# Kernel optimization log

Measured on AMD Instinct MI355X. Metric: run time of the kernel, lower is better.

The kernel has to match this reference:

```python
import jax, jax.numpy as jnp
import numpy as np

BATCH, IN, HID, OMID, OUT = 8192, 64, 1024, 128, 1
MAX_ITER = 8
EPS = 1e-3


def setup_inputs() -> dict:
    key = jax.random.key(0)
    ks = jax.random.split(key, 32)
    s_in, s_h = 1.0 / np.sqrt(IN), 1.0 / np.sqrt(HID)
    d = {"x": jax.random.normal(ks[0], (BATCH, IN), jnp.float32)}
    names = ["i", "f", "c", "o"]
    for j, n in enumerate(names):
        d[f"Wx{n}"] = jax.random.uniform(ks[1 + 4 * j], (HID, IN), jnp.float32, -s_in, s_in)
        d[f"bx{n}"] = jax.random.uniform(ks[2 + 4 * j], (HID,), jnp.float32, -s_in, s_in)
        d[f"Wh{n}"] = jax.random.uniform(ks[3 + 4 * j], (HID, HID), jnp.float32, -s_h, s_h)
        d[f"bh{n}"] = jax.random.uniform(ks[4 + 4 * j], (HID,), jnp.float32, -s_h, s_h)
    d["W_halt"] = jax.random.uniform(ks[20], (1, HID), jnp.float32, -s_h, s_h)
    d["b_halt"] = jax.random.uniform(ks[21], (1,), jnp.float32, -s_h, s_h)
    d["W1"] = jax.random.uniform(ks[22], (OMID, HID), jnp.float32, -s_h, s_h)
    d["b1"] = jax.random.uniform(ks[23], (OMID,), jnp.float32, -s_h, s_h)
    s_m = 1.0 / np.sqrt(OMID)
    d["W2"] = jax.random.uniform(ks[24], (OUT, OMID), jnp.float32, -s_m, s_m)
    d["b2"] = jax.random.uniform(ks[25], (OUT,), jnp.float32, -s_m, s_m)
    return d


def _act_forward(x, Wxi, bxi, Whi, bhi, Wxf, bxf, Whf, bhf, Wxc, bxc, Whc, bhc,
                 Wxo, bxo, Who, bho, W_halt, b_halt, W1, b1, W2, b2):
    B = x.shape[0]
    state0 = jnp.zeros((B, HID), x.dtype)
    cell0 = jnp.zeros((B, HID), x.dtype)
    p0 = jnp.zeros((B,), x.dtype)
    active0 = jnp.ones((B,), bool)

    def step(carry, t):
        state, cell, p_sum, active = carry
        # four LSTM-style gates (computed dense; masked update == torch's gather/scatter)
        i_g = jax.nn.sigmoid(x @ Wxi.T + bxi + state @ Whi.T + bhi)
        f_g = jax.nn.sigmoid(x @ Wxf.T + bxf + state @ Whf.T + bhf)
        c_g = jnp.tanh(x @ Wxc.T + bxc + state @ Whc.T + bhc)
        o_g = jax.nn.sigmoid(x @ Wxo.T + bxo + state @ Who.T + bho)
        am = active[:, None]
        cell = jnp.where(am, f_g * cell + i_g * c_g, cell)
        state = jnp.where(am, o_g * jnp.tanh(cell), state)
        out = jax.nn.sigmoid(jax.nn.relu(state @ W1.T + b1) @ W2.T + b2)  # (B, OUT)
        h = jax.nn.sigmoid(state @ W_halt.T + b_halt)[:, 0]               # (B,)
        p_new = p_sum + h
        last = t == MAX_ITER - 1
        finished = active & ((p_new >= 1.0 - EPS) | last)
        halt_rec = jnp.where(finished, 1.0 - p_sum, jnp.where(active, h, 0.0))
        p_sum = jnp.where(finished, 1.0, jnp.where(active, p_new, p_sum))
        out_rec = jnp.where(am, out, 0.0)
        active = active & ~finished
        return (state, cell, p_sum, active), (out_rec, halt_rec)

    _, (outs, halts) = jax.lax.scan(step, (state0, cell0, p0, active0), jnp.arange(MAX_ITER))
    # outs: (T, B, OUT), halts: (T, B); final = sum_t out_t * p_halt_t
    return jnp.einsum("tbo,tb->bo", outs, halts)


def reference(x, Wxi, bxi, Whi, bhi, Wxf, bxf, Whf, bhf, Wxc, bxc, Whc, bhc,
              Wxo, bxo, Who, bho, W_halt, b_halt, W1, b1, W2, b2):
    return _act_forward(x, Wxi, bxi, Whi, bhi, Wxf, bxf, Whf, bhf, Wxc, bxc, Whc, bhc,
                        Wxo, bxo, Who, bho, W_halt, b_halt, W1, b1, W2, b2)
```

## Files before the change

### kernel.cpp

```cpp
#include <hip/hip_runtime.h>
#include <hip/hip_bf16.h>

#define BATCH 8192
#define IN_DIM 64
#define HID 1024
#define KTOT 1088
#define NGATES 4096
#define OMID 128
#define NP 256
#define MAX_ITER 8

#define TM 128
#define TN 128
#define TK 64
#define GTM 256
#define GTN 256
#define TAILB 64

typedef __attribute__((ext_vector_type(8))) short short8;
typedef __attribute__((ext_vector_type(4))) float float4v;

__device__ __forceinline__ float bf2f(short s) {
    union { float f; unsigned u; } v; v.u = ((unsigned)(unsigned short)s) << 16; return v.f;
}
__device__ __forceinline__ short f2bf(float f) {
    union { float f; unsigned u; } v; v.f = f;
    unsigned r = v.u + 0x7fff + ((v.u >> 16) & 1);
    return (short)(r >> 16);
}
__device__ __forceinline__ float sigmoidf_(float x) {
    float xc = fminf(fmaxf(x, -30.f), 30.f);
    return 1.f / (1.f + __expf(-xc));
}
__device__ __forceinline__ float tanhf_(float x) {
    float xc = fminf(fmaxf(x, -15.f), 15.f);
    float e = __expf(2.f * xc);
    return (e - 1.f) / (e + 1.f);
}
__device__ __forceinline__ int aload(const int* p) {
    return __hip_atomic_load((int*)p, __ATOMIC_RELAXED, __HIP_MEMORY_SCOPE_AGENT);
}
__device__ __forceinline__ void astore(int* p, int v) {
    __hip_atomic_store(p, v, __ATOMIC_RELAXED, __HIP_MEMORY_SCOPE_AGENT);
}

__device__ __forceinline__ void gbar(int* bar, int phase, int tid) {
    __syncthreads();
    if (tid == 0) {
        __threadfence();
        __hip_atomic_fetch_add(bar, 1, __ATOMIC_ACQ_REL, __HIP_MEMORY_SCOPE_AGENT);
        while (aload(bar) < TAILB * phase)
            __builtin_amdgcn_s_sleep(8);
        __threadfence();
    }
    __syncthreads();
}

__device__ __forceinline__ void gates_epilogue(
    const float4v (&acc)[4][4], int m0, int bx, int wave, int lane, int first,
    const float* __restrict__ bias_g, float* __restrict__ cell,
    short* __restrict__ Sout, const int* __restrict__ ridx, int n_act)
{
    const int wm = wave & 1, wn = wave >> 1;
    const int colq = lane & 15, q = lane >> 4;
    const int G = bx * 2 + wn;
    const int h = G * 16 + colq;
    const float bi  = bias_g[G * 64 +  0 + colq];
    const float bff = bias_g[G * 64 + 16 + colq];
    const float bc  = bias_g[G * 64 + 32 + colq];
    const float bo  = bias_g[G * 64 + 48 + colq];
#pragma unroll
    for (int i = 0; i < 4; ++i) {
        const int pbase = m0 + wm * 64 + i * 16 + q * 4;
#pragma unroll
        for (int r = 0; r < 4; ++r) {
            const int pos = pbase + r;
            if (pos < n_act) {
                const int row = ridx[pos];
                const float ig = sigmoidf_(acc[i][0][r] + bi);
                const float fg = sigmoidf_(acc[i][1][r] + bff);
                const float cg = tanhf_(acc[i][2][r] + bc);
                const float og = sigmoidf_(acc[i][3][r] + bo);
                const size_t ci = (size_t)row * HID + h;
                const float c = first ? (ig * cg) : (fg * cell[ci] + ig * cg);
                cell[ci] = c;
                Sout[(size_t)row * HID + h] = f2bf(og * tanhf_(c));
            }
        }
    }
}

__global__ __launch_bounds__(512, 1) void gates_k(
    const short* __restrict__ S, const short* __restrict__ XB,
    const short* __restrict__ B,
    const float* __restrict__ bias_g, int nK, int hidK, int first,
    float* __restrict__ cell, short* __restrict__ Sout,
    const int* __restrict__ ridx, const int* __restrict__ cnt, int t)
{
    __shared__ short As[2][GTM * TK];
    __shared__ short Bs[2][GTN * TK];
    const int n_act = cnt[t];
    const int tid  = threadIdx.x;
    const int wave = tid >> 6, lane = tid & 63;
    const int wm2 = wave >> 2, wn4 = wave & 3;
    const int colq = lane & 15, q = lane >> 4;
    const int lrow8 = lane >> 3;
    const int lk    = (((lane & 7) ^ lrow8) * 8);
    const int xq = colq & 7;
    const int abase = (wm2 * 128 + colq) * TK;
    const int bbase = (wn4 * 64  + colq) * TK;

    int bx, byS;
    {
        const int lin  = (int)blockIdx.x + 16 * (int)blockIdx.y;
        const int xcd  = lin & 7;
        const int slot = lin >> 3;
        bx  = (xcd & 1) * 8 + (slot & 7);
        byS = (xcd >> 1) * 4 + (slot >> 3);
    }
    const int n0 = bx * GTN;

    for (int by = byS; by * GTM < n_act; by += 16) {
        const int m0 = by * GTM;

        int rows_[4];
        const short* gb[4];
#pragma unroll
        for (int it = 0; it < 4; ++it) {
            const int rr = wave * 32 + it * 8 + lrow8;
            rows_[it] = ridx[m0 + rr];
            gb[it] = B + (size_t)(n0 + rr) * KTOT + lk;
        }

        float4v acc[8][4];
#pragma unroll
        for (int i = 0; i < 8; ++i)
#pragma unroll
            for (int j = 0; j < 4; ++j) acc[i][j] = (float4v)0.f;

        auto stage = [&](int ki, int buf) {
            const int kk = ki * TK;
            const bool fromS = (kk < hidK);
#pragma unroll
            for (int it = 0; it < 4; ++it) {
                const int dst = (wave * 32 + it * 8) * TK;
                const short* sa = fromS
                    ? (S  + (size_t)rows_[it] * HID    + kk + lk)
                    : (XB + (size_t)rows_[it] * IN_DIM + lk);
                __builtin_amdgcn_global_load_lds(
                    (const __attribute__((address_space(1))) void*)sa,
                    (__attribute__((address_space(3))) void*)(As[buf] + dst), 16, 0, 0);
                __builtin_amdgcn_global_load_lds(
                    (const __attribute__((address_space(1))) void*)(gb[it] + kk),
                    (__attribute__((address_space(3))) void*)(Bs[buf] + dst), 16, 0, 0);
            }
        };

        stage(0, 0);
        if (nK > 1) {
            stage(1, 1);
            asm volatile("s_waitcnt vmcnt(16)" ::: "memory");
        } else {
            asm volatile("s_waitcnt vmcnt(0)" ::: "memory");
        }
        asm volatile("s_barrier" ::: "memory");

        for (int ki = 0; ki < nK; ++ki) {
            const int cur = ki & 1;
            const short* Ac = As[cur];
            const short* Bc = Bs[cur];
#pragma unroll
            for (int c2 = 0; c2 < 2; ++c2) {
                const int xt = ((q + 4 * c2) ^ xq) << 3;
                short8 af[8], bf[4];
#pragma unroll
                for (int i = 0; i < 8; ++i)
                    af[i] = *(const short8*)(Ac + abase + i * (16 * TK) + xt);
#pragma unroll
                for (int j = 0; j < 4; ++j)
                    bf[j] = *(const short8*)(Bc + bbase + j * (16 * TK) + xt);
#pragma unroll
                for (int i = 0; i < 8; ++i)
#pragma unroll
                    for (int j = 0; j < 4; ++j)
                        acc[i][j] = __builtin_amdgcn_mfma_f32_16x16x32_bf16(af[i], bf[j], acc[i][j], 0, 0, 0);
            }
            asm volatile("s_waitcnt lgkmcnt(0)" ::: "memory");
            asm volatile("s_barrier" ::: "memory");
            if (ki + 2 < nK) {
                stage(ki + 2, cur);
                asm volatile("s_waitcnt vmcnt(16)" ::: "memory");
                asm volatile("s_barrier" ::: "memory");
            } else if (ki + 1 < nK) {
                asm volatile("s_waitcnt vmcnt(0)" ::: "memory");
                asm volatile("s_barrier" ::: "memory");
            }
        }

        const int G = bx * 4 + wn4;
        const int h = G * 16 + colq;
        const float bi  = bias_g[G * 64 +  0 + colq];
        const float bff = bias_g[G * 64 + 16 + colq];
        const float bc  = bias_g[G * 64 + 32 + colq];
        const float bo  = bias_g[G * 64 + 48 + colq];
#pragma unroll
        for (int i = 0; i < 8; ++i) {
            const int pbase = m0 + wm2 * 128 + i * 16 + q * 4;
#pragma unroll
            for (int r = 0; r < 4; ++r) {
                const int pos = pbase + r;
                if (pos < n_act) {
                    const int row = ridx[pos];
                    const float ig = sigmoidf_(acc[i][0][r] + bi);
                    const float fg = sigmoidf_(acc[i][1][r] + bff);
                    const float cg = tanhf_(acc[i][2][r] + bc);
                    const float og = sigmoidf_(acc[i][3][r] + bo);
                    const size_t ci = (size_t)row * HID + h;
                    const float c = first ? (ig * cg) : (fg * cell[ci] + ig * cg);
                    cell[ci] = c;
                    Sout[(size_t)row * HID + h] = f2bf(og * tanhf_(c));
                }
            }
        }
    }
}

__device__ __forceinline__ void gates_tile(
    short* As, short* Bs, int tid,
    const short* __restrict__ S, const short* __restrict__ XB,
    const short* __restrict__ B,
    const float* __restrict__ bias_g,
    float* __restrict__ cell, short* __restrict__ Sout,
    const int* __restrict__ ridx, int n_act, int m0, int bx)
{
    const int wave = tid >> 6, lane = tid & 63;
    const int wm = wave & 1, wn = wave >> 1;
    const int colq = lane & 15, q = lane >> 4;
    const int lrow8 = lane >> 3;
    const int lk    = (((lane & 7) ^ lrow8) * 8);
    const int n0 = bx * TN;

    int aoff[4][2], boff[4][2];
#pragma unroll
    for (int i = 0; i < 4; ++i) {
        const int Ra = wm * 64 + i * 16 + colq;
        const int Rb = wn * 64 + i * 16 + colq;
#pragma unroll
        for (int c2 = 0; c2 < 2; ++c2) {
            const int C = q + 4 * c2;
            aoff[i][c2] = Ra * TK + ((C ^ (Ra & 7)) << 3);
            boff[i][c2] = Rb * TK + ((C ^ (Rb & 7)) << 3);
        }
    }

    float4v acc[4][4];
#pragma unroll
    for (int i = 0; i < 4; ++i)
#pragma unroll
        for (int j = 0; j < 4; ++j) acc[i][j] = (float4v)0.f;

    const short* gaS[4];
    const short* gaX[4];
    const short* gb[4];
#pragma unroll
    for (int it = 0; it < 4; ++it) {
        const int rr = (wave * 4 + it) * 8;
        const int r0 = ridx[m0 + rr + lrow8];
        gaS[it] = S + (size_t)r0 * HID + lk;
        gaX[it] = XB + (size_t)r0 * IN_DIM + lk;
        gb[it]  = B + (size_t)(n0 + rr + lrow8) * KTOT + lk;
    }

    for (int ki = 0; ki < KTOT / TK; ++ki) {
        const bool fromS = (ki * TK < HID);
#pragma unroll
        for (int it = 0; it < 4; ++it) {
            const int rr = (wave * 4 + it) * 8;
            const short* a0 = fromS ? gaS[it] : gaX[it];
            __builtin_amdgcn_global_load_lds(
                (const __attribute__((address_space(1))) void*)a0,
                (__attribute__((address_space(3))) void*)(As + rr * TK), 16, 0, 0);
            __builtin_amdgcn_global_load_lds(
                (const __attribute__((address_space(1))) void*)gb[it],
                (__attribute__((address_space(3))) void*)(Bs + rr * TK), 16, 0, 0);
            gaS[it] += TK; gb[it] += TK;
        }
        __syncthreads();
#pragma unroll
        for (int c2 = 0; c2 < 2; ++c2) {
            short8 af[4], bf[4];
#pragma unroll
            for (int i = 0; i < 4; ++i) {
                af[i] = *(const short8*)(As + aoff[i][c2]);
                bf[i] = *(const short8*)(Bs + boff[i][c2]);
            }
#pragma unroll
            for (int i = 0; i < 4; ++i)
#pragma unroll
                for (int j = 0; j < 4; ++j)
                    acc[i][j] = __builtin_amdgcn_mfma_f32_16x16x32_bf16(af[i], bf[j], acc[i][j], 0, 0, 0);
        }
        __syncthreads();
    }

    gates_epilogue(acc, m0, bx, wave, lane, 0, bias_g, cell, Sout, ridx, n_act);
    __syncthreads();
}

__device__ __forceinline__ void midfin_tile(
    short* As, short* Bs, int tid,
    const short* __restrict__ Snew, const short* __restrict__ P,
    const float* __restrict__ bias_p, const float* __restrict__ W_halt,
    const float* __restrict__ W2, const float* __restrict__ b2,
    float* __restrict__ outp, float* __restrict__ p_sum,
    const int* __restrict__ rprev, int* __restrict__ rnext,
    int* __restrict__ cnt, int t, int m0, int n_act)
{
    const int wave = tid >> 6, lane = tid & 63;
    const int wm = wave & 1, wn = wave >> 1;
    const int colq = lane & 15, q = lane >> 4;
    const int lrow8 = lane >> 3;
    const int lk    = (((lane & 7) ^ lrow8) * 8);

    float4v acc[4][4];
#pragma unroll
    for (int i = 0; i < 4; ++i)
#pragma unroll
        for (int j = 0; j < 4; ++j) acc[i][j] = (float4v)0.f;

    const short* ga[4];
    const short* gb[4];
#pragma unroll
    for (int it = 0; it < 4; ++it) {
        const int rr = (wave * 4 + it) * 8;
        ga[it] = Snew + (size_t)rprev[m0 + rr + lrow8] * HID + lk;
        gb[it] = P + (size_t)(rr + lrow8) * HID + lk;
    }
    int aoff[4][2], boff[4][2];
#pragma unroll
    for (int i = 0; i < 4; ++i) {
        const int Ra = wm * 64 + i * 16 + colq;
        const int Rb = wn * 64 + i * 16 + colq;
#pragma unroll
        for (int c2 = 0; c2 < 2; ++c2) {
            const int C = q + 4 * c2;
            aoff[i][c2] = Ra * TK + ((C ^ (Ra & 7)) << 3);
            boff[i][c2] = Rb * TK + ((C ^ (Rb & 7)) << 3);
        }
    }

    for (int k0 = 0; k0 < HID; k0 += TK) {
#pragma unroll
        for (int it = 0; it < 4; ++it) {
            const int rr = (wave * 4 + it) * 8;
            __builtin_amdgcn_global_load_lds(
                (const __attribute__((address_space(1))) void*)ga[it],
                (__attribute__((address_space(3))) void*)(As + rr * TK), 16, 0, 0);
            __builtin_amdgcn_global_load_lds(
                (const __attribute__((address_space(1))) void*)gb[it],
                (__attribute__((address_space(3))) void*)(Bs + rr * TK), 16, 0, 0);
            ga[it] += TK; gb[it] += TK;
        }
        __syncthreads();
#pragma unroll
        for (int c2 = 0; c2 < 2; ++c2) {
            short8 af[4], bf[4];
#pragma unroll
            for (int i = 0; i < 4; ++i) {
                af[i] = *(const short8*)(As + aoff[i][c2]);
                bf[i] = *(const short8*)(Bs + boff[i][c2]);
            }
#pragma unroll
            for (int i = 0; i < 4; ++i)
#pragma unroll
                for (int j = 0; j < 4; ++j)
                    acc[i][j] = __builtin_amdgcn_mfma_f32_16x16x32_bf16(af[i], bf[j], acc[i][j], 0, 0, 0);
        }
        __syncthreads();
    }

    float* red  = (float*)As;
    float* hbuf = ((float*)As) + 256;

    for (int s = 0; s < 32; ++s) {
        const int lr = wave * 32 + s;
        const int row = rprev[m0 + lr];
        const short* Ar = Snew + (size_t)row * HID + lane * 16;
        const short8 v0 = *(const short8*)Ar;
        const short8 v1 = *(const short8*)(Ar + 8);
        const float* Wh = W_halt + lane * 16;
        float hv = 0.f;
#pragma unroll
        for (int e = 0; e < 8; ++e) hv += bf2f(v0[e]) * Wh[e];
#pragma unroll
        for (int e = 0; e < 8; ++e) hv += bf2f(v1[e]) * Wh[8 + e];
#pragma unroll
        for (int o = 32; o > 0; o >>= 1) hv += __shfl_down(hv, o);
        if (lane == 0) hbuf[lr] = hv;
    }

    float pr[4][4];
#pragma unroll
    for (int i = 0; i < 4; ++i)
#pragma unroll
        for (int r = 0; r < 4; ++r) pr[i][r] = 0.f;
#pragma unroll
    for (int j = 0; j < 4; ++j) {
        const int col = wn * 64 + j * 16 + colq;
        const float b = bias_p[col];
        const float w2 = W2[col];
#pragma unroll
        for (int i = 0; i < 4; ++i)
#pragma unroll
            for (int r = 0; r < 4; ++r)
                pr[i][r] += fmaxf(acc[i][j][r] + b, 0.f) * w2;
    }
#pragma unroll
    for (int i = 0; i < 4; ++i)
#pragma unroll
        for (int r = 0; r < 4; ++r) {
            float v = pr[i][r];
            v += __shfl_down(v, 8, 16);
            v += __shfl_down(v, 4, 16);
            v += __shfl_down(v, 2, 16);
            v += __shfl_down(v, 1, 16);
            if (colq == 0)
                red[((((wn * 2) + wm) * 4 + i) * 4 + q) * 4 + r] = v;
        }
    __syncthreads();

    if (tid < TM) {
        const int pos = m0 + tid;
        if (pos < n_act) {
            const int lwm = tid >> 6, i = (tid >> 4) & 3, lq = (tid >> 2) & 3, r = tid & 3;
            const float odot = red[((lwm * 4 + i) * 4 + lq) * 4 + r]
                             + red[(((2 + lwm) * 4 + i) * 4 + lq) * 4 + r];
            const int row = rprev[pos];
            const float ov = sigmoidf_(odot + b2[0]);
            const float h  = sigmoidf_(hbuf[tid] + bias_p[OMID]);
            const float ps = p_sum[row];
            const float pn = ps + h;
            const bool fin = (pn >= 1.f - 1e-3f) || (t == MAX_ITER - 1);
            const float halt = fin ? (1.f - ps) : h;
            outp[row] += ov * halt;
            p_sum[row] = fin ? 1.f : pn;
            if (!fin) {
                const int d = atomicAdd(&cnt[t + 1], 1);
                astore(&rnext[d], row);
            }
        }
    }
    __syncthreads();
}

__global__ __launch_bounds__(256) void midfin_k(
    const short* __restrict__ Snew, const short* __restrict__ P,
    const float* __restrict__ bias_p, const float* __restrict__ W_halt,
    const float* __restrict__ W2, const float* __restrict__ b2,
    float* __restrict__ outp, float* __restrict__ p_sum,
    const int* __restrict__ rprev, int* __restrict__ rnext,
    int* __restrict__ cnt, int t)
{
    __shared__ short As[TM * TK];
    __shared__ short Bs[TN * TK];
    const int n_act = cnt[t];
    for (int tile = blockIdx.x; tile * TM < n_act; tile += gridDim.x)
        midfin_tile(As, Bs, threadIdx.x, Snew, P, bias_p, W_halt, W2, b2,
                    outp, p_sum, rprev, rnext, cnt, t, tile * TM, n_act);
}

__global__ __launch_bounds__(256) void tail_k(
    const short* __restrict__ Wg, const float* __restrict__ bias_g,
    const short* __restrict__ P, const float* __restrict__ bias_p,
    const float* __restrict__ W_halt, const float* __restrict__ W2,
    const float* __restrict__ b2,
    short* __restrict__ S0, short* __restrict__ S1,
    const short* __restrict__ XB,
    float* __restrict__ cell, float* __restrict__ outp,
    float* __restrict__ p_sum,
    int* __restrict__ ridx0, int* __restrict__ ridx1,
    int* __restrict__ cnt, int* __restrict__ bar)
{
    __shared__ short As[TM * TK];
    __shared__ short Bs[TN * TK];
    const int tid = threadIdx.x;
    int phase = 0;
    int t = 2;
    while (true) {
        short* Snew = (t & 1) ? S0 : S1;
        const int* rprev = (t & 1) ? ridx1 : ridx0;
        int* rnext = (t & 1) ? ridx0 : ridx1;
        const int n = aload(&cnt[t]);
        for (int tile = blockIdx.x; tile * TM < n; tile += gridDim.x)
            midfin_tile(As, Bs, tid, Snew, P, bias_p, W_halt, W2, b2,
                        outp, p_sum, rprev, rnext, cnt, t, tile * TM, n);
        if (t == MAX_ITER - 1) break;
        ++phase; gbar(bar, phase, tid);
        const int n1 = aload(&cnt[t + 1]);
        if (n1 == 0) break;
        {
            short* Sot = (t & 1) ? S1 : S0;
            const int ntiles = ((n1 + TM - 1) / TM) * (NGATES / TN);
            for (int e = blockIdx.x; e < ntiles; e += gridDim.x)
                gates_tile(As, Bs, tid, Snew, XB, Wg, bias_g, cell, Sot,
                           rnext, n1, (e >> 5) * TM, e & 31);
        }
        ++phase; gbar(bar, phase, tid);
        ++t;
    }
}

#define SETUP_XB    (BATCH * IN_DIM)
#define SETUP_WG    (NGATES * KTOT)
#define SETUP_P     (NP * HID)
#define SETUP_TOT   (SETUP_XB + SETUP_WG + SETUP_P)
__global__ __launch_bounds__(256) void setup_k(
    const float* __restrict__ x,
    const float* __restrict__ Whi, const float* __restrict__ Whf,
    const float* __restrict__ Whc, const float* __restrict__ Who,
    const float* __restrict__ Wxi, const float* __restrict__ Wxf,
    const float* __restrict__ Wxc, const float* __restrict__ Wxo,
    const float* __restrict__ bxi, const float* __restrict__ bhi,
    const float* __restrict__ bxf, const float* __restrict__ bhf,
    const float* __restrict__ bxc, const float* __restrict__ bhc,
    const float* __restrict__ bxo, const float* __restrict__ bho,
    const float* __restrict__ W1, const float* __restrict__ b1,
    const float* __restrict__ W_halt, const float* __restrict__ b_halt,
    short* __restrict__ XB,
    float* __restrict__ p_sum,
    int* __restrict__ ridx0, int* __restrict__ ridx1, int* __restrict__ cnt,
    int* __restrict__ bar, float* __restrict__ outp,
    short* __restrict__ Wg, float* __restrict__ bias_g,
    short* __restrict__ P, float* __restrict__ bias_p)
{
    int idx = blockIdx.x * 256 + threadIdx.x;
    if (idx < SETUP_XB) {
        const int row = idx >> 6, k = idx & 63;
        XB[idx] = f2bf(x[idx]);
        if (k == 0) {
            p_sum[row] = 0.f;
            outp[row] = 0.f;
            ridx0[row] = row;
            ridx1[row] = 0;
        }
        if (row == 0 && k <= MAX_ITER) cnt[k] = (k == 0) ? BATCH : 0;
        if (row == 1 && k == 0) bar[0] = 0;
        return;
    }
    idx -= SETUP_XB;
    if (idx < SETUP_WG) {
        const int n = idx / KTOT, k = idx - n * KTOT;
        const int G = n >> 6, g = (n >> 4) & 3, q = n & 15;
        const int h = G * 16 + q;
        const float* Wh = (g == 0) ? Whi : (g == 1) ? Whf : (g == 2) ? Whc : Who;
        const float* Wx = (g == 0) ? Wxi : (g == 1) ? Wxf : (g == 2) ? Wxc : Wxo;
        const float v = (k < HID) ? Wh[h * HID + k] : Wx[h * IN_DIM + (k - HID)];
        Wg[idx] = f2bf(v);
        if (k == 0) {
            const float* bx = (g == 0) ? bxi : (g == 1) ? bxf : (g == 2) ? bxc : bxo;
            const float* bh = (g == 0) ? bhi : (g == 1) ? bhf : (g == 2) ? bhc : bho;
            bias_g[n] = bx[h] + bh[h];
        }
        return;
    }
    idx -= SETUP_WG;
    if (idx < SETUP_P) {
        const int n = idx >> 10, k = idx & 1023;
        const float v = (n < OMID) ? W1[n * HID + k] : (n == OMID ? W_halt[k] : 0.f);
        P[idx] = f2bf(v);
        if (k == 0) bias_p[n] = (n < OMID) ? b1[n] : (n == OMID ? b_halt[0] : 0.f);
    }
}

extern "C" void kernel_launch(void* const* d_in, const int* in_sizes, int n_in,
                              void* d_out, int out_size, void* d_ws, size_t ws_size,
                              hipStream_t stream) {
    const float* x    = (const float*)d_in[0];
    const float* Wxi  = (const float*)d_in[1];
    const float* bxi  = (const float*)d_in[2];
    const float* Whi  = (const float*)d_in[3];
    const float* bhi  = (const float*)d_in[4];
    const float* Wxf  = (const float*)d_in[5];
    const float* bxf  = (const float*)d_in[6];
    const float* Whf  = (const float*)d_in[7];
    const float* bhf  = (const float*)d_in[8];
    const float* Wxc  = (const float*)d_in[9];
    const float* bxc  = (const float*)d_in[10];
    const float* Whc  = (const float*)d_in[11];
    const float* bhc  = (const float*)d_in[12];
    const float* Wxo  = (const float*)d_in[13];
    const float* bxo  = (const float*)d_in[14];
    const float* Who  = (const float*)d_in[15];
    const float* bho  = (const float*)d_in[16];
    const float* W_halt = (const float*)d_in[17];
    const float* b_halt = (const float*)d_in[18];
    const float* W1   = (const float*)d_in[19];
    const float* b1   = (const float*)d_in[20];
    const float* W2   = (const float*)d_in[21];
    const float* b2   = (const float*)d_in[22];

    char* p = (char*)d_ws;
    auto carve = [&](size_t bytes) { char* r = p; p += (bytes + 255) & ~(size_t)255; return r; };
    short* S0     = (short*)carve((size_t)BATCH * HID * 2);
    short* S1     = (short*)carve((size_t)BATCH * HID * 2);
    short* XB     = (short*)carve((size_t)BATCH * IN_DIM * 2);
    short* Wg     = (short*)carve((size_t)NGATES * KTOT * 2);
    float* bias_g = (float*)carve((size_t)NGATES * 4);
    short* P      = (short*)carve((size_t)NP * HID * 2);
    float* bias_p = (float*)carve((size_t)NP * 4);
    float* cell   = (float*)carve((size_t)BATCH * HID * 4);
    float* p_sum  = (float*)carve((size_t)BATCH * 4);
    int*   ridx0  = (int*)carve((size_t)BATCH * 4);
    int*   ridx1  = (int*)carve((size_t)BATCH * 4);
    int*   cnt    = (int*)carve((size_t)(MAX_ITER + 1) * 4);
    int*   bar    = (int*)carve(256);
    float* outp   = (float*)d_out;

    setup_k<<<(SETUP_TOT + 255) / 256, 256, 0, stream>>>(
        x, Whi, Whf, Whc, Who, Wxi, Wxf, Wxc, Wxo,
        bxi, bhi, bxf, bhf, bxc, bhc, bxo, bho,
        W1, b1, W_halt, b_halt,
        XB, p_sum, ridx0, ridx1, cnt, bar, outp,
        Wg, bias_g, P, bias_p);

    gates_k<<<dim3(NGATES / GTN, 16), 512, 0, stream>>>(
        S0, XB, Wg + HID, bias_g, 1, 0, 1, cell, S1, ridx0, cnt, 0);
    midfin_k<<<64, 256, 0, stream>>>(
        S1, P, bias_p, W_halt, W2, b2, outp, p_sum, ridx0, ridx1, cnt, 0);
    gates_k<<<dim3(NGATES / GTN, 16), 512, 0, stream>>>(
        S1, XB, Wg, bias_g, KTOT / TK, HID, 0, cell, S0, ridx1, cnt, 1);
    midfin_k<<<64, 256, 0, stream>>>(
        S0, P, bias_p, W_halt, W2, b2, outp, p_sum, ridx1, ridx0, cnt, 1);
    gates_k<<<dim3(NGATES / GTN, 16), 512, 0, stream>>>(
        S0, XB, Wg, bias_g, KTOT / TK, HID, 0, cell, S1, ridx0, cnt, 2);
    tail_k<<<TAILB, 256, 0, stream>>>(
        Wg, bias_g, P, bias_p, W_halt, W2, b2,
        S0, S1, XB, cell, outp, p_sum, ridx0, ridx1, cnt, bar);
}
```

Baseline: 477.3 us.

## Split gate GEMM K-loop into four interleaved phases with staggered loads and setprio

Reorganizes the gate GEMM main loop into four sub-phases that each compute half of the B columns for half of the K tile. Global-to-LDS loads of the next B tile and the tile after next for A are issued between the phases, and each MFMA cluster is raised with s_setprio and fenced with sched_barrier. The goal is to overlap the gathered A/B global loads with MFMA work more finely, in the style of a ping-pong schedule, instead of one bulk stage after every K step. The cost is many more barriers per iteration and trickier vmcnt accounting. The launch grid literal is rewritten (16 equals NGATES/GTN), which has no effect.

```diff
diff --git a/kernel.cpp b/kernel.cpp
--- a/kernel.cpp
+++ b/kernel.cpp
@@ -123,14 +123,16 @@
     for (int by = byS; by * GTM < n_act; by += 16) {
         const int m0 = by * GTM;
 
-        int rows_[4];
-        const short* gb[4];
-#pragma unroll
-        for (int it = 0; it < 4; ++it) {
-            const int rr = wave * 32 + it * 8 + lrow8;
-            rows_[it] = ridx[m0 + rr];
-            gb[it] = B + (size_t)(n0 + rr) * KTOT + lk;
-        }
+        int arow[2][2];
+        const short* bptr[2][2];
+#pragma unroll
+        for (int h = 0; h < 2; ++h)
+#pragma unroll
+            for (int l = 0; l < 2; ++l) {
+                const int rr = h * 128 + wave * 16 + l * 8 + lrow8;
+                arow[h][l] = ridx[m0 + rr];
+                bptr[h][l] = B + (size_t)(n0 + rr) * KTOT + lk;
+            }
 
         float4v acc[8][4];
 #pragma unroll
@@ -138,63 +140,115 @@
 #pragma unroll
             for (int j = 0; j < 4; ++j) acc[i][j] = (float4v)0.f;
 
-        auto stage = [&](int ki, int buf) {
-            const int kk = ki * TK;
+        auto stageA = [&](int kt, int h) {
+            const int kk = kt * TK;
             const bool fromS = (kk < hidK);
 #pragma unroll
-            for (int it = 0; it < 4; ++it) {
-                const int dst = (wave * 32 + it * 8) * TK;
+            for (int l = 0; l < 2; ++l) {
+                const int dst = (h * 128 + wave * 16 + l * 8) * TK;
                 const short* sa = fromS
-                    ? (S  + (size_t)rows_[it] * HID    + kk + lk)
-                    : (XB + (size_t)rows_[it] * IN_DIM + lk);
+                    ? (S  + (size_t)arow[h][l] * HID    + kk + lk)
+                    : (XB + (size_t)arow[h][l] * IN_DIM + lk);
                 __builtin_amdgcn_global_load_lds(
                     (const __attribute__((address_space(1))) void*)sa,
-                    (__attribute__((address_space(3))) void*)(As[buf] + dst), 16, 0, 0);
+                    (__attribute__((address_space(3))) void*)(As[kt & 1] + dst), 16, 0, 0);
+            }
+        };
+        auto stageB = [&](int kt, int h) {
+            const int kk = kt * TK;
+#pragma unroll
+            for (int l = 0; l < 2; ++l) {
+                const int dst = (h * 128 + wave * 16 + l * 8) * TK;
                 __builtin_amdgcn_global_load_lds(
-                    (const __attribute__((address_space(1))) void*)(gb[it] + kk),
-                    (__attribute__((address_space(3))) void*)(Bs[buf] + dst), 16, 0, 0);
+                    (const __attribute__((address_space(1))) void*)(bptr[h][l] + kk),
+                    (__attribute__((address_space(3))) void*)(Bs[kt & 1] + dst), 16, 0, 0);
             }
         };
 
-        stage(0, 0);
+        stageA(0, 0); stageA(0, 1); stageB(0, 0); stageB(0, 1);
         if (nK > 1) {
-            stage(1, 1);
-            asm volatile("s_waitcnt vmcnt(16)" ::: "memory");
+            stageA(1, 0); stageA(1, 1);
+            asm volatile("s_waitcnt vmcnt(4)" ::: "memory");
         } else {
             asm volatile("s_waitcnt vmcnt(0)" ::: "memory");
         }
         asm volatile("s_barrier" ::: "memory");
 
-        for (int ki = 0; ki < nK; ++ki) {
-            const int cur = ki & 1;
-            const short* Ac = As[cur];
-            const short* Bc = Bs[cur];
-#pragma unroll
-            for (int c2 = 0; c2 < 2; ++c2) {
-                const int xt = ((q + 4 * c2) ^ xq) << 3;
-                short8 af[8], bf[4];
-#pragma unroll
-                for (int i = 0; i < 8; ++i)
-                    af[i] = *(const short8*)(Ac + abase + i * (16 * TK) + xt);
-#pragma unroll
-                for (int j = 0; j < 4; ++j)
-                    bf[j] = *(const short8*)(Bc + bbase + j * (16 * TK) + xt);
-#pragma unroll
-                for (int i = 0; i < 8; ++i)
-#pragma unroll
-                    for (int j = 0; j < 4; ++j)
-                        acc[i][j] = __builtin_amdgcn_mfma_f32_16x16x32_bf16(af[i], bf[j], acc[i][j], 0, 0, 0);
-            }
+        for (int kt = 0; kt < nK; ++kt) {
+            const short* Ac = As[kt & 1];
+            const short* Bc = Bs[kt & 1];
+            const int xt0 = (q ^ xq) << 3;
+            const int xt1 = ((q + 4) ^ xq) << 3;
+            short8 af[8], bf[4];
+
+#pragma unroll
+            for (int i = 0; i < 8; ++i)
+                af[i] = *(const short8*)(Ac + abase + i * (16 * TK) + xt0);
+            bf[0] = *(const short8*)(Bc + bbase + 0 * (16 * TK) + xt0);
+            bf[1] = *(const short8*)(Bc + bbase + 1 * (16 * TK) + xt0);
+            if (kt + 1 < nK) stageB(kt + 1, 0);
+            asm volatile("s_barrier" ::: "memory");
             asm volatile("s_waitcnt lgkmcnt(0)" ::: "memory");
-            asm volatile("s_barrier" ::: "memory");
-            if (ki + 2 < nK) {
-                stage(ki + 2, cur);
-                asm volatile("s_waitcnt vmcnt(16)" ::: "memory");
-                asm volatile("s_barrier" ::: "memory");
-            } else if (ki + 1 < nK) {
+            __builtin_amdgcn_sched_barrier(0);
+            __builtin_amdgcn_s_setprio(1);
+#pragma unroll
+            for (int i = 0; i < 8; ++i) {
+                acc[i][0] = __builtin_amdgcn_mfma_f32_16x16x32_bf16(af[i], bf[0], acc[i][0], 0, 0, 0);
+                acc[i][1] = __builtin_amdgcn_mfma_f32_16x16x32_bf16(af[i], bf[1], acc[i][1], 0, 0, 0);
+            }
+            __builtin_amdgcn_s_setprio(0);
+            asm volatile("s_barrier" ::: "memory");
+
+            bf[2] = *(const short8*)(Bc + bbase + 2 * (16 * TK) + xt0);
+            bf[3] = *(const short8*)(Bc + bbase + 3 * (16 * TK) + xt0);
+            if (kt + 1 < nK) stageB(kt + 1, 1);
+            asm volatile("s_barrier" ::: "memory");
+            asm volatile("s_waitcnt lgkmcnt(0)" ::: "memory");
+            __builtin_amdgcn_sched_barrier(0);
+            __builtin_amdgcn_s_setprio(1);
+#pragma unroll
+            for (int i = 0; i < 8; ++i) {
+                acc[i][2] = __builtin_amdgcn_mfma_f32_16x16x32_bf16(af[i], bf[2], acc[i][2], 0, 0, 0);
+                acc[i][3] = __builtin_amdgcn_mfma_f32_16x16x32_bf16(af[i], bf[3], acc[i][3], 0, 0, 0);
+            }
+            __builtin_amdgcn_s_setprio(0);
+            asm volatile("s_barrier" ::: "memory");
+
+#pragma unroll
+            for (int i = 0; i < 8; ++i)
+                af[i] = *(const short8*)(Ac + abase + i * (16 * TK) + xt1);
+            bf[0] = *(const short8*)(Bc + bbase + 0 * (16 * TK) + xt1);
+            bf[1] = *(const short8*)(Bc + bbase + 1 * (16 * TK) + xt1);
+            asm volatile("s_barrier" ::: "memory");
+            asm volatile("s_waitcnt lgkmcnt(0)" ::: "memory");
+            __builtin_amdgcn_sched_barrier(0);
+            __builtin_amdgcn_s_setprio(1);
+#pragma unroll
+            for (int i = 0; i < 8; ++i) {
+                acc[i][0] = __builtin_amdgcn_mfma_f32_16x16x32_bf16(af[i], bf[0], acc[i][0], 0, 0, 0);
+                acc[i][1] = __builtin_amdgcn_mfma_f32_16x16x32_bf16(af[i], bf[1], acc[i][1], 0, 0, 0);
+            }
+            __builtin_amdgcn_s_setprio(0);
+            asm volatile("s_barrier" ::: "memory");
+
+            bf[2] = *(const short8*)(Bc + bbase + 2 * (16 * TK) + xt1);
+            bf[3] = *(const short8*)(Bc + bbase + 3 * (16 * TK) + xt1);
+            if (kt + 2 < nK) { stageA(kt + 2, 0); stageA(kt + 2, 1); }
+            asm volatile("s_barrier" ::: "memory");
+            asm volatile("s_waitcnt lgkmcnt(0)" ::: "memory");
+            __builtin_amdgcn_sched_barrier(0);
+            __builtin_amdgcn_s_setprio(1);
+#pragma unroll
+            for (int i = 0; i < 8; ++i) {
+                acc[i][2] = __builtin_amdgcn_mfma_f32_16x16x32_bf16(af[i], bf[2], acc[i][2], 0, 0, 0);
+                acc[i][3] = __builtin_amdgcn_mfma_f32_16x16x32_bf16(af[i], bf[3], acc[i][3], 0, 0, 0);
+            }
+            __builtin_amdgcn_s_setprio(0);
+            if (kt + 2 < nK)
+                asm volatile("s_waitcnt vmcnt(4)" ::: "memory");
+            else
                 asm volatile("s_waitcnt vmcnt(0)" ::: "memory");
-                asm volatile("s_barrier" ::: "memory");
-            }
+            asm volatile("s_barrier" ::: "memory");
         }
 
         const int G = bx * 4 + wn4;
@@ -623,15 +677,15 @@
         XB, p_sum, ridx0, ridx1, cnt, bar, outp,
         Wg, bias_g, P, bias_p);
 
-    gates_k<<<dim3(NGATES / GTN, 16), 512, 0, stream>>>(
+    gates_k<<<dim3(16, 16), 512, 0, stream>>>(
         S0, XB, Wg + HID, bias_g, 1, 0, 1, cell, S1, ridx0, cnt, 0);
     midfin_k<<<64, 256, 0, stream>>>(
         S1, P, bias_p, W_halt, W2, b2, outp, p_sum, ridx0, ridx1, cnt, 0);
-    gates_k<<<dim3(NGATES / GTN, 16), 512, 0, stream>>>(
+    gates_k<<<dim3(16, 16), 512, 0, stream>>>(
         S1, XB, Wg, bias_g, KTOT / TK, HID, 0, cell, S0, ridx1, cnt, 1);
     midfin_k<<<64, 256, 0, stream>>>(
         S0, P, bias_p, W_halt, W2, b2, outp, p_sum, ridx1, ridx0, cnt, 1);
-    gates_k<<<dim3(NGATES / GTN, 16), 512, 0, stream>>>(
+    gates_k<<<dim3(16, 16), 512, 0, stream>>>(
         S0, XB, Wg, bias_g, KTOT / TK, HID, 0, cell, S1, ridx0, cnt, 2);
     tail_k<<<TAILB, 256, 0, stream>>>(
         Wg, bias_g, P, bias_p, W_halt, W2, b2,
```

Result: no change. 474.5 us (-0.6%).
